# Performance work log

Measured on AMD Instinct MI355X. Metric: run time of the kernel, lower is better.

## Reference

```python
import jax, jax.numpy as jnp
import numpy as np

N, E, G, D, L = 200000, 400000, 1024, 300, 5
BN_EPS = 1e-5


def setup_inputs() -> dict:
    key = jax.random.key(0)
    ks = jax.random.split(key, 14)
    s = 0.1  # param init scale
    return {
        "atomic_number": jax.random.randint(ks[0], (N,), 0, 120),
        "chirality_type": jax.random.randint(ks[1], (N,), 0, 3),
        "bond_type": jax.random.randint(ks[2], (E,), 0, 6),
        "bond_direction_type": jax.random.randint(ks[3], (E,), 0, 3),
        "src": jax.random.randint(ks[4], (E,), 0, N),
        "dst": jax.random.randint(ks[5], (E,), 0, N),
        "graph_ids": jnp.sort(jax.random.randint(ks[6], (N,), 0, G)),
        "num_graphs": G,
        "node_emb0": jax.random.normal(ks[7], (120, D), jnp.float32) * s,
        "node_emb1": jax.random.normal(ks[8], (3, D), jnp.float32) * s,
        "edge_emb0": jax.random.normal(ks[9], (L, 6, D), jnp.float32) * s,
        "edge_emb1": jax.random.normal(ks[10], (L, 3, D), jnp.float32) * s,
        "W1": jax.random.normal(ks[11], (L, D, 2 * D), jnp.float32) * (1.0 / np.sqrt(D)),
        "b1": jnp.zeros((L, 2 * D), jnp.float32),
        "W2": jax.random.normal(ks[12], (L, 2 * D, D), jnp.float32) * (1.0 / np.sqrt(2 * D)),
        "b2": jnp.zeros((L, D), jnp.float32),
        "bn_gamma": jnp.ones((L, D), jnp.float32),
        "bn_beta": jnp.zeros((L, D), jnp.float32),
        "bn_mean": jnp.zeros((L, D), jnp.float32),
        "bn_var": jnp.ones((L, D), jnp.float32),
        "Wd": jax.random.normal(ks[13], (D, 256), jnp.float32) * (1.0 / np.sqrt(D)),
        "bd": jnp.zeros((256,), jnp.float32),
    }


def reference(atomic_number, chirality_type, bond_type, bond_direction_type,
              src, dst, graph_ids, num_graphs,
              node_emb0, node_emb1, edge_emb0, edge_emb1,
              W1, b1, W2, b2, bn_gamma, bn_beta, bn_mean, bn_var, Wd, bd):
    n = atomic_number.shape[0]
    # input node embedding: sum of the two categorical lookups
    h = node_emb0[atomic_number] + node_emb1[chirality_type]  # [N, D]
    for l in range(L):
        # per-layer edge embedding (sum of bond-type / bond-direction lookups)
        e = edge_emb0[l][bond_type] + edge_emb1[l][bond_direction_type]  # [E, D]
        # message u_add_e, sum reduce onto destination nodes
        m = h[src] + e
        agg = jax.ops.segment_sum(m, dst, num_segments=n)  # [N, D]
        # GIN MLP: Linear(D,2D) -> ReLU -> Linear(2D,D)
        h = jax.nn.relu(agg @ W1[l] + b1[l]) @ W2[l] + b2[l]
        # BatchNorm1d in eval mode (running stats)
        h = (h - bn_mean[l]) * jax.lax.rsqrt(bn_var[l] + BN_EPS) * bn_gamma[l] + bn_beta[l]
        if l < L - 1:  # ReLU on all but last layer (dropout is identity in eval)
            h = jax.nn.relu(h)
    # AvgPooling over nodes of each graph
    gsum = jax.ops.segment_sum(h, graph_ids, num_segments=num_graphs)  # [G, D]
    cnt = jax.ops.segment_sum(jnp.ones((n, 1), h.dtype), graph_ids, num_segments=num_graphs)
    gavg = gsum / jnp.maximum(cnt, 1.0)
    # head: Dropout (eval identity) + Linear(300, 256), then squeeze (no-op here)
    return jnp.squeeze(gavg @ Wd + bd)
```

## Files before the change

kernel.cpp:

```cpp
#include <hip/hip_runtime.h>
#include <hip/hip_bf16.h>
#include <hip/hip_fp16.h>

#define D 300
#define D2 150
#define HD 600
#define NLAYERS 5
#define BN_EPS 1e-5f

#define KS1 10
#define NT1 5
#define KS2 20
#define NT2 3
#define P1 (NT1*KS1*4096)
#define P2 (NT2*KS2*4096)

#define SCAN_BLK 1024

typedef _Float16 f16x8 __attribute__((ext_vector_type(8)));
typedef __attribute__((ext_vector_type(4))) float f32x4;

__device__ inline ushort f2h(float x) {
    __half h = __float2half(x);
    return *reinterpret_cast<ushort*>(&h);
}
__device__ inline float h2f(ushort u) {
    __half h;
    *reinterpret_cast<ushort*>(&h) = u;
    return __half2float(h);
}
__device__ inline uint pack2h(float lo, float hi) {
    return (uint)f2h(lo) | ((uint)f2h(hi) << 16);
}

__global__ __launch_bounds__(256) void zero_kernel(uint4* __restrict__ p, long n4)
{
    long i = (long)blockIdx.x * blockDim.x + threadIdx.x;
    long stride = (long)gridDim.x * blockDim.x;
    uint4 z = make_uint4(0u, 0u, 0u, 0u);
    for (; i < n4; i += stride) p[i] = z;
}

__global__ __launch_bounds__(256) void embed_kernel(
    const int* __restrict__ an, const int* __restrict__ ch,
    const float* __restrict__ e0, const float* __restrict__ e1,
    uint* __restrict__ h_u, int N)
{
    int node = blockIdx.x * 4 + (threadIdx.x >> 6);
    if (node >= N) return;
    int lane = threadIdx.x & 63;
    const float* r0 = e0 + (size_t)an[node] * D;
    const float* r1 = e1 + (size_t)ch[node] * D;
    uint* hr = h_u + (size_t)node * D2;
    for (int d2 = lane; d2 < D2; d2 += 64) {
        float2 a = *(const float2*)(r0 + d2 * 2);
        float2 b = *(const float2*)(r1 + d2 * 2);
        hr[d2] = pack2h(a.x + b.x, a.y + b.y);
    }
}

__global__ __launch_bounds__(256) void count_kernel(
    const int* __restrict__ dst, int* __restrict__ deg, int E)
{
    int e = blockIdx.x * 256 + threadIdx.x;
    if (e < E) atomicAdd(&deg[dst[e]], 1);
}

__global__ __launch_bounds__(256) void scan_part_kernel(
    const int* __restrict__ deg, int* __restrict__ part, int N)
{
    __shared__ int sm[256];
    int b = blockIdx.x, t = threadIdx.x;
    int base = b * SCAN_BLK + t * 4;
    int s = 0;
#pragma unroll
    for (int j = 0; j < 4; ++j) { int i = base + j; if (i < N) s += deg[i]; }
    sm[t] = s;
    __syncthreads();
    for (int off = 128; off > 0; off >>= 1) {
        if (t < off) sm[t] += sm[t + off];
        __syncthreads();
    }
    if (t == 0) part[b] = sm[0];
}

__global__ __launch_bounds__(256) void scan_top_kernel(int* __restrict__ part, int NB)
{
    __shared__ int sm[256];
    int t = threadIdx.x;
    int own = (t < NB) ? part[t] : 0;
    sm[t] = own;
    __syncthreads();
    for (int off = 1; off < 256; off <<= 1) {
        int u = (t >= off) ? sm[t - off] : 0;
        __syncthreads();
        sm[t] += u;
        __syncthreads();
    }
    if (t < NB) part[t] = sm[t] - own;
}

__global__ __launch_bounds__(256) void scan_write_kernel(
    const int* __restrict__ deg, const int* __restrict__ part,
    int* __restrict__ offsets, int* __restrict__ cursor, int N, int E)
{
    __shared__ int sm[256];
    int b = blockIdx.x, t = threadIdx.x;
    int base = b * SCAN_BLK + t * 4;
    int v[4], s = 0;
#pragma unroll
    for (int j = 0; j < 4; ++j) { int i = base + j; v[j] = (i < N) ? deg[i] : 0; s += v[j]; }
    int own = s;
    sm[t] = s;
    __syncthreads();
    for (int off = 1; off < 256; off <<= 1) {
        int u = (t >= off) ? sm[t - off] : 0;
        __syncthreads();
        sm[t] += u;
        __syncthreads();
    }
    int ex = sm[t] - own + part[b];
#pragma unroll
    for (int j = 0; j < 4; ++j) {
        int i = base + j;
        if (i < N) { offsets[i] = ex; cursor[i] = ex; ex += v[j]; }
    }
    if (b == 0 && t == 0) offsets[N] = E;
}

__global__ __launch_bounds__(256) void scatter_kernel(
    const int* __restrict__ dst, int* __restrict__ cursor,
    int* __restrict__ csr, int E)
{
    int e = blockIdx.x * 256 + threadIdx.x;
    if (e < E) {
        int pos = atomicAdd(&cursor[dst[e]], 1);
        csr[pos] = e;
    }
}

__global__ __launch_bounds__(256) void eprep_kernel(
    const int* __restrict__ csr, const int* __restrict__ src,
    const int* __restrict__ bt, const int* __restrict__ bd,
    int* __restrict__ esrc, unsigned char* __restrict__ ecomb, int E)
{
    int p = blockIdx.x * 256 + threadIdx.x;
    if (p < E) {
        int e = csr[p];
        esrc[p] = src[e];
        ecomb[p] = (unsigned char)(bt[e] * 3 + bd[e]);
    }
}

__global__ __launch_bounds__(256) void etab_kernel(
    const float* __restrict__ ee0, const float* __restrict__ ee1,
    uint* __restrict__ etab)
{
    int i = blockIdx.x * 256 + threadIdx.x;
    const int total = NLAYERS * 18 * D2;
    if (i >= total) return;
    int d2 = i % D2;
    int rest = i / D2;
    int c = rest % 18, l = rest / 18;
    int btv = c / 3, bdv = c % 3;
    const float* r0 = ee0 + ((size_t)l * 6 + btv) * D + d2 * 2;
    const float* r1 = ee1 + ((size_t)l * 3 + bdv) * D + d2 * 2;
    etab[i] = pack2h(r0[0] + r1[0], r0[1] + r1[1]);
}

__global__ void prep_bn_kernel(
    const float* __restrict__ b2, const float* __restrict__ gamma,
    const float* __restrict__ beta, const float* __restrict__ mean,
    const float* __restrict__ var, float* __restrict__ scale2,
    float* __restrict__ shift2, int n)
{
    int i = blockIdx.x * blockDim.x + threadIdx.x;
    if (i >= n) return;
    float s = gamma[i] * rsqrtf(var[i] + BN_EPS);
    scale2[i] = s;
    shift2[i] = (b2[i] - mean[i]) * s + beta[i];
}

__global__ __launch_bounds__(256) void conv_w_kernel(
    const float* __restrict__ W1, const float* __restrict__ W2,
    ushort* __restrict__ w1h, ushort* __restrict__ w2h)
{
    int i = blockIdx.x * blockDim.x + threadIdx.x;
    const int PER = P1 + P2;
    if (i >= NLAYERS * PER) return;
    int l = i / PER;
    int r = i - l * PER;
    float v;
    ushort* ph;
    if (r < P1) {
        int pos = r;
        int j = pos & 7, c = (pos >> 3) & 127, kg = (pos >> 10) & 3;
        int rest = pos >> 12;
        int ks = rest % KS1, nt = rest / KS1;
        int k = ks * 32 + kg * 8 + j, n = nt * 128 + c;
        v = (k < D && n < HD) ? W1[(size_t)l * D * HD + (size_t)k * HD + n] : 0.f;
        ph = w1h + (size_t)l * P1 + pos;
    } else {
        int pos = r - P1;
        int j = pos & 7, c = (pos >> 3) & 127, kg = (pos >> 10) & 3;
        int rest = pos >> 12;
        int ks = rest % KS2, nt = rest / KS2;
        int k = ks * 32 + kg * 8 + j, n = nt * 128 + c;
        v = (k < HD && n < D) ? W2[(size_t)l * HD * D + (size_t)k * D + n] : 0.f;
        ph = w2h + (size_t)l * P2 + pos;
    }
    *ph = f2h(v);
}

template<bool RELU2>
__global__ __launch_bounds__(512, 4) void fused_mlp_kernel(
    const uint* __restrict__ Hin,
    const uint* __restrict__ etab_l,
    const int* __restrict__ esrc, const unsigned char* __restrict__ ecomb,
    const int* __restrict__ offsets,
    const uint4* __restrict__ B1,
    const uint4* __restrict__ B2,
    const float* __restrict__ bias1,
    const float* __restrict__ scale2,
    const float* __restrict__ shift2,
    uint* __restrict__ Hout,
    int M)
{
    __shared__ ushort lds[KS2 * 4 * 64 * 8];

    int t = threadIdx.x;
    int lane = t & 63;
    int wid = t >> 6;
    int lanelo = lane & 15;
    int kg = lane >> 4;
    int m0 = blockIdx.x * 64;

    {
        uint* ldsAu = (uint*)lds;
        int q = lane >> 4;
        int ql = lane & 15;
#pragma unroll
        for (int pass = 0; pass < 2; ++pass) {
            int rowl = wid * 8 + pass * 4 + q;
            int v = m0 + rowl;
            float ax[10], ay[10];
#pragma unroll
            for (int j = 0; j < 10; ++j) { ax[j] = 0.f; ay[j] = 0.f; }
            if (v < M) {
                int p0 = offsets[v], p1 = offsets[v + 1];
                for (int p = p0; p < p1; ++p) {
                    int s = esrc[p];
                    int c = ecomb[p];
                    const uint* hr = Hin + (size_t)s * D2;
                    const uint* er = etab_l + c * D2;
#pragma unroll
                    for (int j = 0; j < 10; ++j) {
                        int d2 = ql + j * 16;
                        if (d2 < D2) {
                            uint hv = hr[d2];
                            uint ev = er[d2];
                            ax[j] += h2f((ushort)(hv & 0xffffu)) + h2f((ushort)(ev & 0xffffu));
                            ay[j] += h2f((ushort)(hv >> 16))     + h2f((ushort)(ev >> 16));
                        }
                    }
                }
            }
#pragma unroll
            for (int j = 0; j < 10; ++j) {
                int d2 = ql + j * 16;
                int qc = d2 >> 2;
                ldsAu[(qc * 64 + (rowl ^ (qc & 7))) * 4 + (d2 & 3)] = pack2h(ax[j], ay[j]);
            }
        }
    }
    __syncthreads();

    {
        f32x4 acc[4][5];
#pragma unroll
        for (int mi = 0; mi < 4; ++mi)
#pragma unroll
            for (int ni = 0; ni < 5; ++ni) {
                f32x4 z = {0.f, 0.f, 0.f, 0.f};
                acc[mi][ni] = z;
            }

        int addrb[5];
#pragma unroll
        for (int ni = 0; ni < 5; ++ni) {
            int col = wid * 80 + ni * 16 + lanelo;
            int nt = col >> 7, c = col & 127;
            addrb[ni] = nt * (KS1 * 512) + kg * 128 + c;
        }

        uint4 bn[5];
#pragma unroll
        for (int ni = 0; ni < 5; ++ni) bn[ni] = B1[addrb[ni]];

        const f16x8* ap = (const f16x8*)lds;
#pragma unroll
        for (int ks = 0; ks < KS1; ++ks) {
            uint4 bc[5];
#pragma unroll
            for (int ni = 0; ni < 5; ++ni) bc[ni] = bn[ni];
            if (ks + 1 < KS1) {
#pragma unroll
                for (int ni = 0; ni < 5; ++ni) bn[ni] = B1[addrb[ni] + (ks + 1) * 512];
            }
            int q1 = ks * 4 + kg;
            int ab = q1 * 64 + (lanelo ^ (q1 & 7));
            f16x8 a0 = ap[ab];
            f16x8 a1 = ap[ab + 16];
            f16x8 a2 = ap[ab + 32];
            f16x8 a3 = ap[ab + 48];
#pragma unroll
            for (int ni = 0; ni < 5; ++ni) {
                f16x8 b = *(const f16x8*)&bc[ni];
                acc[0][ni] = __builtin_amdgcn_mfma_f32_16x16x32_f16(a0, b, acc[0][ni], 0, 0, 0);
                acc[1][ni] = __builtin_amdgcn_mfma_f32_16x16x32_f16(a1, b, acc[1][ni], 0, 0, 0);
                acc[2][ni] = __builtin_amdgcn_mfma_f32_16x16x32_f16(a2, b, acc[2][ni], 0, 0, 0);
                acc[3][ni] = __builtin_amdgcn_mfma_f32_16x16x32_f16(a3, b, acc[3][ni], 0, 0, 0);
            }
        }

        __syncthreads();

        uint* ldsHu = (uint*)lds;
#pragma unroll
        for (int ni = 0; ni < 5; ++ni) {
            int col = wid * 80 + ni * 16 + lanelo;
            float bias = (col < HD) ? bias1[col] : 0.f;
            int ks2 = col >> 5, g2 = (col >> 3) & 3, j2 = col & 7;
            int dbase = (ks2 * 4 + g2) * 256 + (j2 >> 1);
#pragma unroll
            for (int mi = 0; mi < 4; ++mi) {
                int r0 = mi * 16 + kg * 4;
#pragma unroll
                for (int r = 0; r < 4; ++r) {
                    float y = fmaxf(acc[mi][ni][r] + bias, 0.f);
                    float yn = __shfl_xor(y, 1);
                    if ((lanelo & 1) == 0)
                        ldsHu[dbase + (r0 + r) * 4] = pack2h(y, yn);
                }
            }
        }
    }
    __syncthreads();

    {
        f32x4 acc[4][3];
#pragma unroll
        for (int mi = 0; mi < 4; ++mi)
#pragma unroll
            for (int ni = 0; ni < 3; ++ni) {
                f32x4 z = {0.f, 0.f, 0.f, 0.f};
                acc[mi][ni] = z;
            }

        int addrb[3];
#pragma unroll
        for (int ni = 0; ni < 3; ++ni) {
            int col = wid * 48 + ni * 16 + lanelo;
            int nt = col >> 7, c = col & 127;
            addrb[ni] = nt * (KS2 * 512) + kg * 128 + c;
        }

        uint4 bn0[3], bn1[3];
#pragma unroll
        for (int ni = 0; ni < 3; ++ni) bn0[ni] = B2[addrb[ni]];
#pragma unroll
        for (int ni = 0; ni < 3; ++ni) bn1[ni] = B2[addrb[ni] + 512];

        const f16x8* hp = (const f16x8*)lds;
#pragma unroll
        for (int ks = 0; ks < KS2; ++ks) {
            uint4 bc[3];
#pragma unroll
            for (int ni = 0; ni < 3; ++ni) bc[ni] = bn0[ni];
#pragma unroll
            for (int ni = 0; ni < 3; ++ni) bn0[ni] = bn1[ni];
            {
                int nk = (ks + 2 < KS2) ? ks + 2 : KS2 - 1;
#pragma unroll
                for (int ni = 0; ni < 3; ++ni) bn1[ni] = B2[addrb[ni] + nk * 512];
            }
            int ab = (ks * 4 + kg) * 64 + lanelo;
            f16x8 a0 = hp[ab];
            f16x8 a1 = hp[ab + 16];
            f16x8 a2 = hp[ab + 32];
            f16x8 a3 = hp[ab + 48];
#pragma unroll
            for (int ni = 0; ni < 3; ++ni) {
                f16x8 b = *(const f16x8*)&bc[ni];
                acc[0][ni] = __builtin_amdgcn_mfma_f32_16x16x32_f16(a0, b, acc[0][ni], 0, 0, 0);
                acc[1][ni] = __builtin_amdgcn_mfma_f32_16x16x32_f16(a1, b, acc[1][ni], 0, 0, 0);
                acc[2][ni] = __builtin_amdgcn_mfma_f32_16x16x32_f16(a2, b, acc[2][ni], 0, 0, 0);
                acc[3][ni] = __builtin_amdgcn_mfma_f32_16x16x32_f16(a3, b, acc[3][ni], 0, 0, 0);
            }
        }

        __syncthreads();

        uint* stg = (uint*)lds;
#pragma unroll
        for (int ni = 0; ni < 3; ++ni) {
            int col = wid * 48 + ni * 16 + lanelo;
            float sc = 1.f, sh = 0.f;
            if (col < D) { sc = scale2[col]; sh = shift2[col]; }
#pragma unroll
            for (int mi = 0; mi < 4; ++mi) {
                int r0 = mi * 16 + kg * 4;
#pragma unroll
                for (int r = 0; r < 4; ++r) {
                    float y = acc[mi][ni][r] * sc + sh;
                    if (RELU2) y = fmaxf(y, 0.f);
                    float yn = __shfl_xor(y, 1);
                    if ((lanelo & 1) == 0 && col < D)
                        stg[(r0 + r) * 154 + (col >> 1)] = pack2h(y, yn);
                }
            }
        }
    }
    __syncthreads();

    {
        const uint* stg = (const uint*)lds;
#pragma unroll
        for (int i = 0; i < 19; ++i) {
            int g = t + i * 512;
            if (g < 64 * 150) {
                int row = g / 150, c = g - row * 150;
                if (m0 + row < M)
                    Hout[(size_t)(m0 + row) * D2 + c] = stg[row * 154 + c];
            }
        }
    }
}

__global__ __launch_bounds__(320) void pool_kernel(
    const ushort* __restrict__ h, const int* __restrict__ gid,
    float* __restrict__ gavg, int N)
{
    int g = blockIdx.x;
    int lo = 0, hi = N;
    while (lo < hi) { int mid = (lo + hi) >> 1; if (gid[mid] < g) lo = mid + 1; else hi = mid; }
    int start = lo;
    lo = start; hi = N;
    while (lo < hi) { int mid = (lo + hi) >> 1; if (gid[mid] <= g) lo = mid + 1; else hi = mid; }
    int end = lo;
    int d = threadIdx.x;
    if (d >= D) return;
    float s = 0.f;
    for (int i = start; i < end; ++i) s += h2f(h[(size_t)i * D + d]);
    float cnt = (float)(end - start);
    gavg[(size_t)g * D + d] = s / fmaxf(cnt, 1.f);
}

__global__ __launch_bounds__(256) void head_kernel(
    const float* __restrict__ gavg, const float* __restrict__ Wd,
    const float* __restrict__ bd, float* __restrict__ out)
{
    int g = blockIdx.x;
    int j = threadIdx.x;
    float s = bd[j];
    const float* gr = gavg + (size_t)g * D;
    for (int d = 0; d < D; ++d) s = fmaf(gr[d], Wd[(size_t)d * 256 + j], s);
    out[(size_t)g * 256 + j] = s;
}

extern "C" void kernel_launch(void* const* d_in, const int* in_sizes, int n_in,
                              void* d_out, int out_size, void* d_ws, size_t ws_size,
                              hipStream_t stream)
{
    const int*   atomic_number = (const int*)d_in[0];
    const int*   chirality     = (const int*)d_in[1];
    const int*   bond_type     = (const int*)d_in[2];
    const int*   bond_dir      = (const int*)d_in[3];
    const int*   src           = (const int*)d_in[4];
    const int*   dst           = (const int*)d_in[5];
    const int*   graph_ids     = (const int*)d_in[6];
    const float* node_emb0     = (const float*)d_in[8];
    const float* node_emb1     = (const float*)d_in[9];
    const float* edge_emb0     = (const float*)d_in[10];
    const float* edge_emb1     = (const float*)d_in[11];
    const float* W1            = (const float*)d_in[12];
    const float* b1            = (const float*)d_in[13];
    const float* W2            = (const float*)d_in[14];
    const float* b2            = (const float*)d_in[15];
    const float* bn_gamma      = (const float*)d_in[16];
    const float* bn_beta       = (const float*)d_in[17];
    const float* bn_mean       = (const float*)d_in[18];
    const float* bn_var        = (const float*)d_in[19];
    const float* Wd            = (const float*)d_in[20];
    const float* bd            = (const float*)d_in[21];

    int N = in_sizes[0];
    int E = in_sizes[2];
    int G = out_size / 256;
    float* out = (float*)d_out;

    char* ws = (char*)d_ws;
    size_t offs = 0;
    auto take = [&](size_t nbytes) -> char* {
        char* p = ws + offs;
        offs += (nbytes + 255) & ~(size_t)255;
        return p;
    };
    ushort* w1h    = (ushort*)take((size_t)NLAYERS * P1 * 2);
    ushort* w2h    = (ushort*)take((size_t)NLAYERS * P2 * 2);
    uint*   h0     = (uint*)take((size_t)N * D2 * 4);
    uint*   h1     = (uint*)take((size_t)N * D2 * 4);
    int*    deg    = (int*)take((size_t)N * 4);
    int*    offsets= (int*)take((size_t)(N + 1) * 4);
    int*    cursor = (int*)take((size_t)N * 4);
    int*    csr    = (int*)take((size_t)E * 4);
    int*    esrc   = (int*)take((size_t)E * 4);
    unsigned char* ecomb = (unsigned char*)take((size_t)E);
    uint*   etab   = (uint*)take((size_t)NLAYERS * 18 * D2 * 4);
    int*    part   = (int*)take((size_t)256 * 4);
    float*  gavg   = (float*)take((size_t)G * D * 4);
    float*  scale2 = (float*)take((size_t)NLAYERS * D * 4);
    float*  shift2 = (float*)take((size_t)NLAYERS * D * 4);

    prep_bn_kernel<<<(NLAYERS * D + 255) / 256, 256, 0, stream>>>(
        b2, bn_gamma, bn_beta, bn_mean, bn_var, scale2, shift2, NLAYERS * D);
    {
        int T = NLAYERS * (P1 + P2);
        conv_w_kernel<<<(T + 255) / 256, 256, 0, stream>>>(W1, W2, w1h, w2h);
    }
    etab_kernel<<<(NLAYERS * 18 * D2 + 255) / 256, 256, 0, stream>>>(
        edge_emb0, edge_emb1, etab);
    embed_kernel<<<(N + 3) / 4, 256, 0, stream>>>(
        atomic_number, chirality, node_emb0, node_emb1, h0, N);

    int NB = (N + SCAN_BLK - 1) / SCAN_BLK;
    zero_kernel<<<(int)(((size_t)N + 1023) / 1024), 256, 0, stream>>>((uint4*)deg, (long)N / 4);
    count_kernel<<<(E + 255) / 256, 256, 0, stream>>>(dst, deg, E);
    scan_part_kernel<<<NB, 256, 0, stream>>>(deg, part, N);
    scan_top_kernel<<<1, 256, 0, stream>>>(part, NB);
    scan_write_kernel<<<NB, 256, 0, stream>>>(deg, part, offsets, cursor, N, E);
    scatter_kernel<<<(E + 255) / 256, 256, 0, stream>>>(dst, cursor, csr, E);
    eprep_kernel<<<(E + 255) / 256, 256, 0, stream>>>(csr, src, bond_type, bond_dir, esrc, ecomb, E);

    int mlp_grid = (N + 63) / 64;
    for (int l = 0; l < NLAYERS; ++l) {
        const uint* hin = (l & 1) ? h1 : h0;
        uint* hout      = (l & 1) ? h0 : h1;
        if (l < NLAYERS - 1)
            fused_mlp_kernel<true><<<mlp_grid, 512, 0, stream>>>(
                hin, etab + (size_t)l * 18 * D2, esrc, ecomb, offsets,
                (const uint4*)(w1h + (size_t)l * P1),
                (const uint4*)(w2h + (size_t)l * P2),
                b1 + (size_t)l * HD,
                scale2 + (size_t)l * D, shift2 + (size_t)l * D,
                hout, N);
        else
            fused_mlp_kernel<false><<<mlp_grid, 512, 0, stream>>>(
                hin, etab + (size_t)l * 18 * D2, esrc, ecomb, offsets,
                (const uint4*)(w1h + (size_t)l * P1),
                (const uint4*)(w2h + (size_t)l * P2),
                b1 + (size_t)l * HD,
                scale2 + (size_t)l * D, shift2 + (size_t)l * D,
                hout, N);
    }

    pool_kernel<<<G, 320, 0, stream>>>((const ushort*)h1, graph_ids, gavg, N);
    head_kernel<<<G, 256, 0, stream>>>(gavg, Wd, bd, out);
}
```

Before: 1.680 ms.

## Batch edge gathers by four, double-prefetch B1 tiles, raise MFMA wave priority

The aggregation loop now loads up to four edges' indices and feature rows together, so more gather loads are in flight at once. Each h+e pair is added as packed half2 before it is widened to float. The first GEMM's B-operand prefetch goes from one k-step ahead to two, matching the second GEMM. Both MFMA loops are wrapped in s_setprio so waves issuing matrix ops get scheduling priority. The costs are more registers, and the half-precision add adds a little rounding.

```diff
diff --git a/kernel.cpp b/kernel.cpp
--- a/kernel.cpp
+++ b/kernel.cpp
@@ -248,21 +248,34 @@
             for (int j = 0; j < 10; ++j) { ax[j] = 0.f; ay[j] = 0.f; }
             if (v < M) {
                 int p0 = offsets[v], p1 = offsets[v + 1];
-                for (int p = p0; p < p1; ++p) {
-                    int s = esrc[p];
-                    int c = ecomb[p];
-                    const uint* hr = Hin + (size_t)s * D2;
-                    const uint* er = etab_l + c * D2;
+                int p = p0;
+                while (p < p1) {
+                    int nb = p1 - p; if (nb > 4) nb = 4;
+                    int sa[4], ca[4];
+                    sa[0] = esrc[p];     ca[0] = ecomb[p];
+                    sa[1] = (nb > 1) ? esrc[p + 1] : 0; ca[1] = (nb > 1) ? ecomb[p + 1] : 0;
+                    sa[2] = (nb > 2) ? esrc[p + 2] : 0; ca[2] = (nb > 2) ? ecomb[p + 2] : 0;
+                    sa[3] = (nb > 3) ? esrc[p + 3] : 0; ca[3] = (nb > 3) ? ecomb[p + 3] : 0;
 #pragma unroll
                     for (int j = 0; j < 10; ++j) {
                         int d2 = ql + j * 16;
                         if (d2 < D2) {
-                            uint hv = hr[d2];
-                            uint ev = er[d2];
-                            ax[j] += h2f((ushort)(hv & 0xffffu)) + h2f((ushort)(ev & 0xffffu));
-                            ay[j] += h2f((ushort)(hv >> 16))     + h2f((ushort)(ev >> 16));
+#pragma unroll
+                            for (int i = 0; i < 4; ++i) {
+                                if (i < nb) {
+                                    uint hv = Hin[(size_t)sa[i] * D2 + d2];
+                                    uint ev = etab_l[ca[i] * D2 + d2];
+                                    __half2 hh = *reinterpret_cast<__half2*>(&hv);
+                                    __half2 ee = *reinterpret_cast<__half2*>(&ev);
+                                    __half2 ss = __hadd2(hh, ee);
+                                    float2 f = __half22float2(ss);
+                                    ax[j] += f.x;
+                                    ay[j] += f.y;
+                                }
+                            }
                         }
                     }
+                    p += nb;
                 }
             }
 #pragma unroll
@@ -293,19 +306,24 @@
             addrb[ni] = nt * (KS1 * 512) + kg * 128 + c;
         }
 
-        uint4 bn[5];
-#pragma unroll
-        for (int ni = 0; ni < 5; ++ni) bn[ni] = B1[addrb[ni]];
+        uint4 bn0[5], bn1[5];
+#pragma unroll
+        for (int ni = 0; ni < 5; ++ni) bn0[ni] = B1[addrb[ni]];
+#pragma unroll
+        for (int ni = 0; ni < 5; ++ni) bn1[ni] = B1[addrb[ni] + 512];
 
         const f16x8* ap = (const f16x8*)lds;
 #pragma unroll
         for (int ks = 0; ks < KS1; ++ks) {
             uint4 bc[5];
 #pragma unroll
-            for (int ni = 0; ni < 5; ++ni) bc[ni] = bn[ni];
-            if (ks + 1 < KS1) {
-#pragma unroll
-                for (int ni = 0; ni < 5; ++ni) bn[ni] = B1[addrb[ni] + (ks + 1) * 512];
+            for (int ni = 0; ni < 5; ++ni) bc[ni] = bn0[ni];
+#pragma unroll
+            for (int ni = 0; ni < 5; ++ni) bn0[ni] = bn1[ni];
+            {
+                int nk = (ks + 2 < KS1) ? ks + 2 : KS1 - 1;
+#pragma unroll
+                for (int ni = 0; ni < 5; ++ni) bn1[ni] = B1[addrb[ni] + nk * 512];
             }
             int q1 = ks * 4 + kg;
             int ab = q1 * 64 + (lanelo ^ (q1 & 7));
@@ -313,6 +331,7 @@
             f16x8 a1 = ap[ab + 16];
             f16x8 a2 = ap[ab + 32];
             f16x8 a3 = ap[ab + 48];
+            __builtin_amdgcn_s_setprio(1);
 #pragma unroll
             for (int ni = 0; ni < 5; ++ni) {
                 f16x8 b = *(const f16x8*)&bc[ni];
@@ -321,6 +340,7 @@
                 acc[2][ni] = __builtin_amdgcn_mfma_f32_16x16x32_f16(a2, b, acc[2][ni], 0, 0, 0);
                 acc[3][ni] = __builtin_amdgcn_mfma_f32_16x16x32_f16(a3, b, acc[3][ni], 0, 0, 0);
             }
+            __builtin_amdgcn_s_setprio(0);
         }
 
         __syncthreads();
@@ -389,6 +409,7 @@
             f16x8 a1 = hp[ab + 16];
             f16x8 a2 = hp[ab + 32];
             f16x8 a3 = hp[ab + 48];
+            __builtin_amdgcn_s_setprio(1);
 #pragma unroll
             for (int ni = 0; ni < 3; ++ni) {
                 f16x8 b = *(const f16x8*)&bc[ni];
@@ -397,6 +418,7 @@
                 acc[2][ni] = __builtin_amdgcn_mfma_f32_16x16x32_f16(a2, b, acc[2][ni], 0, 0, 0);
                 acc[3][ni] = __builtin_amdgcn_mfma_f32_16x16x32_f16(a3, b, acc[3][ni], 0, 0, 0);
             }
+            __builtin_amdgcn_s_setprio(0);
         }
 
         __syncthreads();
```

Result: slower. 5.996 ms (+256.9%).
